# Kernel optimization log

Measured on AMD Instinct MI355X. Metric: run time of the kernel, lower is better.

## Reference

```python
import jax, jax.numpy as jnp
import numpy as np

N = 50000      # num nodes
E = 1_200_000  # num edges
NID = 92       # node_input_dim
ED = 1         # edge_input_dim
H = 64         # hidden_dim
L = 5          # num_layers
EMB = 64       # embedding_dim
G = 256        # num graphs in batch
EPS = 1e-5


def _glorot(key, shape):
    fan_in, fan_out = shape[-2], shape[-1]
    lim = float(np.sqrt(6.0 / (fan_in + fan_out)))
    return jax.random.uniform(key, shape, jnp.float32, -lim, lim)


def setup_inputs() -> dict:
    key = jax.random.key(0)
    ks = jax.random.split(key, 16)
    inp = {
        "x": jax.random.normal(ks[0], (N, NID), jnp.float32),
        "edge_attr": jax.random.uniform(ks[1], (E, ED), jnp.float32),
        "edge_index": jax.random.randint(ks[2], (2, E), 0, N, jnp.int32),
        "batch": jnp.sort(jax.random.randint(ks[3], (N,), 0, G, jnp.int32)),
        # node embedding
        "node_W": _glorot(ks[4], (NID, H)),
        "node_b": jnp.zeros((H,), jnp.float32),
        # per-layer message net: Linear(2H+ED,H) -> BN -> SiLU -> Linear(H,H)
        "msg_W1": _glorot(ks[5], (L, 2 * H + ED, H)),
        "msg_b1": jnp.zeros((L, H), jnp.float32),
        "msg_g1": jnp.ones((L, H), jnp.float32),
        "msg_be1": jnp.zeros((L, H), jnp.float32),
        "msg_W2": _glorot(ks[6], (L, H, H)),
        "msg_b2": jnp.zeros((L, H), jnp.float32),
        # per-layer update net: Linear(2H,H) -> BN -> SiLU
        "upd_W": _glorot(ks[7], (L, 2 * H, H)),
        "upd_b": jnp.zeros((L, H), jnp.float32),
        "upd_g": jnp.ones((L, H), jnp.float32),
        "upd_be": jnp.zeros((L, H), jnp.float32),
        # output projection
        "out_W": _glorot(ks[8], (H, EMB)),
        "out_b": jnp.zeros((EMB,), jnp.float32),
    }
    return inp


def _bn(z, g, b):
    # BatchNorm1d, training-mode batch statistics (biased variance), eps=1e-5
    mu = jnp.mean(z, axis=0)
    var = jnp.var(z, axis=0)
    return (z - mu) * jax.lax.rsqrt(var + EPS) * g + b


def reference(x, edge_attr, node_W, node_b, msg_W1, msg_b1, msg_g1, msg_be1,
              msg_W2, msg_b2, upd_W, upd_b, upd_g, upd_be, out_W, out_b,
              edge_index, batch):
    src, dst = edge_index[0], edge_index[1]  # PyG: x_j = x[src], x_i = x[dst]
    h = x @ node_W + node_b                  # [N, H]
    deg = jax.ops.segment_sum(jnp.ones((E,), h.dtype), dst, num_segments=N)
    deg = jnp.maximum(deg, 1.0)[:, None]     # mean aggregation denominator
    for l in range(L):
        # message: cat([x_i, x_j, edge_attr]) -> Linear -> BN -> SiLU -> Linear
        m = jnp.concatenate([h[dst], h[src], edge_attr], axis=1)  # [E, 2H+ED]
        m = _bn(m @ msg_W1[l] + msg_b1[l], msg_g1[l], msg_be1[l])
        m = jax.nn.silu(m) @ msg_W2[l] + msg_b2[l]                # [E, H]
        # aggregate: scatter-mean to destination nodes
        agg = jax.ops.segment_sum(m, dst, num_segments=N) / deg   # [N, H]
        # update: cat([x, agg]) -> Linear -> BN -> SiLU
        u = jnp.concatenate([h, agg], axis=1) @ upd_W[l] + upd_b[l]
        h = jax.nn.silu(_bn(u, upd_g[l], upd_be[l]))              # [N, H]
    # global mean pool over graphs
    cnt = jnp.maximum(jax.ops.segment_sum(jnp.ones((N,), h.dtype), batch, num_segments=G), 1.0)
    g = jax.ops.segment_sum(h, batch, num_segments=G) / cnt[:, None]  # [G, H]
    return jax.nn.silu(g @ out_W + out_b)                              # [G, EMB]
```

## Files before the change

kernel.cpp:

```cpp
#include <hip/hip_runtime.h>
#include <hip/hip_bf16.h>

#define NN 50000
#define EE 1200000
#define GG 256
#define LL 5

__device__ __forceinline__ float silu_f(float x) {
    return x * __builtin_amdgcn_rcpf(1.0f + __expf(-x));
}
__device__ __forceinline__ int rfl(int x) { return __builtin_amdgcn_readfirstlane(x); }

__global__ __launch_bounds__(256) void k_hist(const int* __restrict__ ei, int* __restrict__ fill, int E) {
    int e = blockIdx.x * 256 + threadIdx.x;
    if (e < E) atomicAdd(&fill[ei[E + e]], 1);
}

__global__ __launch_bounds__(256) void k_scan_blk(int* __restrict__ fill, int* __restrict__ rowptr,
                                                  float* __restrict__ degf, int* __restrict__ bsum, int n) {
    __shared__ int wsum[4];
    int tid = threadIdx.x, lane = tid & 63, wid = tid >> 6;
    int i = blockIdx.x * 256 + tid;
    int v = (i < n) ? fill[i] : 0;
    int x = v;
    #pragma unroll
    for (int off = 1; off < 64; off <<= 1) {
        int t = __shfl_up(x, off);
        if (lane >= off) x += t;
    }
    if (lane == 63) wsum[wid] = x;
    __syncthreads();
    int waveoff = 0;
    if (wid > 0) waveoff += wsum[0];
    if (wid > 1) waveoff += wsum[1];
    if (wid > 2) waveoff += wsum[2];
    int inc = x + waveoff;
    if (i < n) {
        rowptr[i + 1] = inc;
        degf[i] = (float)(v > 0 ? v : 1);
        fill[i] = 0;
    }
    if (tid == 255) bsum[blockIdx.x] = inc;
}

__global__ __launch_bounds__(256) void k_scan_top(int* __restrict__ bsum, int B) {
    __shared__ int wsum[4];
    int tid = threadIdx.x, lane = tid & 63, wid = tid >> 6;
    int v = (tid < B) ? bsum[tid] : 0;
    int x = v;
    #pragma unroll
    for (int off = 1; off < 64; off <<= 1) {
        int t = __shfl_up(x, off);
        if (lane >= off) x += t;
    }
    if (lane == 63) wsum[wid] = x;
    __syncthreads();
    int waveoff = 0;
    if (wid > 0) waveoff += wsum[0];
    if (wid > 1) waveoff += wsum[1];
    if (wid > 2) waveoff += wsum[2];
    if (tid < B) bsum[tid] = x + waveoff;
}

__global__ __launch_bounds__(256) void k_scan_add(const int* __restrict__ bsum, int* __restrict__ rowptr, int n) {
    int b = blockIdx.x;
    int i = b * 256 + threadIdx.x;
    if (i < n) {
        int add = (b > 0) ? bsum[b - 1] : 0;
        rowptr[i + 1] += add;
    }
    if (i == 0) rowptr[0] = 0;
}

__global__ __launch_bounds__(256) void k_scatter(const int* __restrict__ ei, const float* __restrict__ ea,
                                                 const int* __restrict__ rowptr, int* __restrict__ fill,
                                                 unsigned int* __restrict__ edata, int E) {
    int e = blockIdx.x * 256 + threadIdx.x;
    if (e < E) {
        int d = ei[E + e];
        int pos = atomicAdd(&fill[d], 1);
        int idx = rowptr[d] + pos;
        int ea15 = (int)(ea[e] * 32768.0f + 0.5f);
        if (ea15 > 32767) ea15 = 32767;
        edata[idx] = ((unsigned int)ea15 << 17) | (unsigned int)ei[e];
    }
}

__global__ __launch_bounds__(256) void k_fold(const float* __restrict__ msg_W2, const float* __restrict__ msg_b2,
                                              const float* __restrict__ upd_W, float* __restrict__ W2p,
                                              float* __restrict__ b2p) {
    int l = blockIdx.x;
    const float* W2 = msg_W2 + (size_t)l * 4096;
    const float* U2 = upd_W + (size_t)l * 8192 + 4096;
    int lane = threadIdx.x & 63, wid = threadIdx.x >> 6;
    for (int ii = 0; ii < 16; ii++) {
        int i = rfl(wid * 16 + ii);
        float acc = 0.0f;
        for (int k = 0; k < 64; k++) acc = fmaf(W2[i * 64 + k], U2[k * 64 + lane], acc);
        W2p[(size_t)l * 4096 + i * 64 + lane] = acc;
    }
    if (wid == 0) {
        float acc = 0.0f;
        for (int k = 0; k < 64; k++) acc = fmaf(msg_b2[l * 64 + k], U2[k * 64 + lane], acc);
        b2p[l * 64 + lane] = acc;
    }
}

__global__ __launch_bounds__(256) void k_node_emb(const float* __restrict__ x, const float* __restrict__ W,
                                                  const float* __restrict__ b, float* __restrict__ h, int n) {
    __shared__ float sW[92 * 64];
    __shared__ float sX[4][736];
    for (int i = threadIdx.x; i < 92 * 64; i += 256) sW[i] = W[i];
    __syncthreads();
    int lane = threadIdx.x & 63, wid = threadIdx.x >> 6;
    int gw = (blockIdx.x * 256 + threadIdx.x) >> 6;
    int nw = (gridDim.x * 256) >> 6;
    float bj = b[lane];
    int tiles = n >> 3;
    for (int t = gw; t < tiles; t += nw) {
        int rb = rfl(t << 3);
        const float4* xb = (const float4*)(x + (size_t)rb * 92);
        float4* sx4 = (float4*)&sX[wid][0];
        sx4[lane] = xb[lane];
        sx4[lane + 64] = xb[lane + 64];
        if (lane < 56) sx4[lane + 128] = xb[lane + 128];
        float acc[8];
        #pragma unroll
        for (int r = 0; r < 8; r++) acc[r] = bj;
        for (int kb = 0; kb < 80; kb += 16) {
            float wv[16];
            #pragma unroll
            for (int t2 = 0; t2 < 16; t2++) wv[t2] = sW[(kb + t2) * 64 + lane];
            #pragma unroll
            for (int r = 0; r < 8; r++) {
                #pragma unroll
                for (int t2 = 0; t2 < 16; t2++) acc[r] = fmaf(sX[wid][r * 92 + kb + t2], wv[t2], acc[r]);
            }
        }
        {
            float wv[12];
            #pragma unroll
            for (int t2 = 0; t2 < 12; t2++) wv[t2] = sW[(80 + t2) * 64 + lane];
            #pragma unroll
            for (int r = 0; r < 8; r++) {
                #pragma unroll
                for (int t2 = 0; t2 < 12; t2++) acc[r] = fmaf(sX[wid][r * 92 + 80 + t2], wv[t2], acc[r]);
            }
        }
        #pragma unroll
        for (int r = 0; r < 8; r++) h[(size_t)(rb + r) * 64 + lane] = acc[r];
    }
}

__global__ __launch_bounds__(256) void k_node_pre(const float* __restrict__ h, const float* __restrict__ W1,
                                                  const float* __restrict__ b1, float* __restrict__ Hd,
                                                  _Float16* __restrict__ Hs, int n) {
    __shared__ float sA[4096], sB[4096];
    __shared__ float sH[4][512];
    for (int i = threadIdx.x; i < 4096; i += 256) { sA[i] = W1[i]; sB[i] = W1[4096 + i]; }
    __syncthreads();
    int lane = threadIdx.x & 63, wid = threadIdx.x >> 6;
    int gw = (blockIdx.x * 256 + threadIdx.x) >> 6;
    int nw = (gridDim.x * 256) >> 6;
    float bj = b1[lane];
    int tiles = n >> 3;
    for (int t = gw; t < tiles; t += nw) {
        int rb = rfl(t << 3);
        const float4* hb = (const float4*)(h + (size_t)rb * 64);
        float4* sh4 = (float4*)&sH[wid][0];
        sh4[lane] = hb[lane];
        sh4[lane + 64] = hb[lane + 64];
        float accA[8], accB[8];
        #pragma unroll
        for (int r = 0; r < 8; r++) { accA[r] = bj; accB[r] = 0.0f; }
        for (int kb = 0; kb < 64; kb += 8) {
            float wA[8], wB[8];
            #pragma unroll
            for (int t2 = 0; t2 < 8; t2++) { wA[t2] = sA[(kb + t2) * 64 + lane]; wB[t2] = sB[(kb + t2) * 64 + lane]; }
            #pragma unroll
            for (int r = 0; r < 8; r++) {
                #pragma unroll
                for (int t2 = 0; t2 < 8; t2++) {
                    float hk = sH[wid][r * 64 + kb + t2];
                    accA[r] = fmaf(hk, wA[t2], accA[r]);
                    accB[r] = fmaf(hk, wB[t2], accB[r]);
                }
            }
        }
        #pragma unroll
        for (int r = 0; r < 8; r++) {
            Hd[(size_t)(rb + r) * 64 + lane] = accA[r];
            Hs[(size_t)(rb + r) * 64 + lane] = (_Float16)accB[r];
        }
    }
}

__global__ __launch_bounds__(256) void k_bn_pre(const float* __restrict__ u, const float* __restrict__ usum,
                                                const float* __restrict__ usq, const float* __restrict__ g,
                                                const float* __restrict__ be, const float* __restrict__ W1,
                                                const float* __restrict__ b1, float* __restrict__ h,
                                                float* __restrict__ Hd, _Float16* __restrict__ Hs,
                                                int n, float invN) {
    __shared__ float sA[4096], sB[4096];
    __shared__ float sH[4][8][64];
    for (int i = threadIdx.x; i < 4096; i += 256) { sA[i] = W1[i]; sB[i] = W1[4096 + i]; }
    __syncthreads();
    int lane = threadIdx.x & 63, wid = threadIdx.x >> 6;
    float mean = usum[lane] * invN;
    float var = usq[lane] * invN - mean * mean;
    float inv = rsqrtf(var + 1e-5f);
    float sc = inv * g[lane];
    float sh = fmaf(-mean, sc, be[lane]);
    float bj = b1[lane];
    int gw = (blockIdx.x * 256 + threadIdx.x) >> 6;
    int nw = (gridDim.x * 256) >> 6;
    int tiles = n >> 3;
    for (int t = gw; t < tiles; t += nw) {
        int rb = rfl(t << 3);
        #pragma unroll
        for (int r = 0; r < 8; r++) {
            float uv = u[(size_t)(rb + r) * 64 + lane];
            float hv = silu_f(fmaf(uv, sc, sh));
            h[(size_t)(rb + r) * 64 + lane] = hv;
            sH[wid][r][lane] = hv;
        }
        float accA[8], accB[8];
        #pragma unroll
        for (int r = 0; r < 8; r++) { accA[r] = bj; accB[r] = 0.0f; }
        for (int k = 0; k < 64; k += 2) {
            float wA0 = sA[k * 64 + lane],       wB0 = sB[k * 64 + lane];
            float wA1 = sA[(k + 1) * 64 + lane], wB1 = sB[(k + 1) * 64 + lane];
            #pragma unroll
            for (int r = 0; r < 8; r++) {
                float h0 = sH[wid][r][k], h1 = sH[wid][r][k + 1];
                accA[r] = fmaf(h0, wA0, accA[r]);
                accB[r] = fmaf(h0, wB0, accB[r]);
                accA[r] = fmaf(h1, wA1, accA[r]);
                accB[r] = fmaf(h1, wB1, accB[r]);
            }
        }
        #pragma unroll
        for (int r = 0; r < 8; r++) {
            Hd[(size_t)(rb + r) * 64 + lane] = accA[r];
            Hs[(size_t)(rb + r) * 64 + lane] = (_Float16)accB[r];
        }
    }
}

__global__ __launch_bounds__(256) void k_edge_stats(const float* __restrict__ Hd, const _Float16* __restrict__ Hs,
                                                    const int* __restrict__ rowptr, const unsigned int* __restrict__ edata,
                                                    const float* __restrict__ w1e,
                                                    float* __restrict__ esum, float* __restrict__ esq, int n) {
    __shared__ float rs[4][64], rq[4][64];
    int wid = threadIdx.x >> 6, lane = threadIdx.x & 63;
    int gw = (blockIdx.x * 256 + threadIdx.x) >> 6;
    int nw = (gridDim.x * 256) >> 6;
    float wj = w1e[lane] * (1.0f / 32768.0f);
    float s = 0.0f, q = 0.0f;
    for (int node = gw; node < n; node += nw) {
        int nu = rfl(node);
        int e0 = rowptr[nu], e1 = rowptr[nu + 1];
        if (e0 == e1) continue;
        float hd = Hd[(size_t)nu * 64 + lane];
        int e = e0;
        for (; e + 16 <= e1; e += 16) {
            float hs[16], av[16];
            #pragma unroll
            for (int j = 0; j < 16; j++) {
                unsigned int p = edata[e + j];
                int sidx = rfl((int)(p & 0x1FFFFu));
                av[j] = (float)rfl((int)(p >> 17));
                hs[j] = (float)Hs[(size_t)sidx * 64 + lane];
            }
            #pragma unroll
            for (int j = 0; j < 16; j++) {
                float z = fmaf(av[j], wj, hd) + hs[j];
                s += z;
                q = fmaf(z, z, q);
            }
        }
        for (; e + 8 <= e1; e += 8) {
            float hs[8], av[8];
            #pragma unroll
            for (int j = 0; j < 8; j++) {
                unsigned int p = edata[e + j];
                int sidx = rfl((int)(p & 0x1FFFFu));
                av[j] = (float)rfl((int)(p >> 17));
                hs[j] = (float)Hs[(size_t)sidx * 64 + lane];
            }
            #pragma unroll
            for (int j = 0; j < 8; j++) {
                float z = fmaf(av[j], wj, hd) + hs[j];
                s += z;
                q = fmaf(z, z, q);
            }
        }
        for (; e < e1; e++) {
            unsigned int p = edata[e];
            int sidx = rfl((int)(p & 0x1FFFFu));
            float a = (float)rfl((int)(p >> 17));
            float z = fmaf(a, wj, hd) + (float)Hs[(size_t)sidx * 64 + lane];
            s += z;
            q = fmaf(z, z, q);
        }
    }
    rs[wid][lane] = s; rq[wid][lane] = q;
    __syncthreads();
    if (wid == 0) {
        float ts = rs[0][lane] + rs[1][lane] + rs[2][lane] + rs[3][lane];
        float tq = rq[0][lane] + rq[1][lane] + rq[2][lane] + rq[3][lane];
        atomicAdd(&esum[lane], ts);
        atomicAdd(&esq[lane], tq);
    }
}

__global__ __launch_bounds__(256) void k_agg_upd(const float* __restrict__ Hd, const _Float16* __restrict__ Hs,
                                                 const int* __restrict__ rowptr, const unsigned int* __restrict__ edata,
                                                 const float* __restrict__ w1e,
                                                 const float* __restrict__ esum, const float* __restrict__ esq,
                                                 const float* __restrict__ g1, const float* __restrict__ be1,
                                                 const float* __restrict__ degf,
                                                 const float* __restrict__ h, const float* __restrict__ U1,
                                                 const float* __restrict__ W2p, const float* __restrict__ b2p,
                                                 const float* __restrict__ ub,
                                                 float* __restrict__ u, float* __restrict__ usum,
                                                 float* __restrict__ usq, int n, float invE) {
    __shared__ float sU[4096], sP[4096];
    __shared__ float2 sHA[4][4][64];
    for (int i = threadIdx.x; i < 4096; i += 256) { sU[i] = U1[i]; sP[i] = W2p[i]; }
    __syncthreads();
    int lane = threadIdx.x & 63, wid = threadIdx.x >> 6;
    float mean = esum[lane] * invE;
    float var = esq[lane] * invE - mean * mean;
    float inv = rsqrtf(var + 1e-5f);
    float sc = inv * g1[lane];
    float sh = fmaf(-mean, sc, be1[lane]);
    float wj = w1e[lane] * (1.0f / 32768.0f);
    float b2j = b2p[lane], ubj = ub[lane];
    int gw = (blockIdx.x * 256 + threadIdx.x) >> 6;
    int nw = (gridDim.x * 256) >> 6;
    float s = 0.0f, q = 0.0f;
    int tiles = n >> 2;
    for (int t = gw; t < tiles; t += nw) {
        int rb = rfl(t << 2);
        float gate[4];
        for (int r = 0; r < 4; r++) {
            int nu = rb + r;
            int e0 = rowptr[nu], e1 = rowptr[nu + 1];
            gate[r] = (e1 > e0) ? 1.0f : 0.0f;
            float hd = Hd[(size_t)nu * 64 + lane];
            float acc = 0.0f;
            int e = e0;
            for (; e + 16 <= e1; e += 16) {
                float hs[16], av[16];
                #pragma unroll
                for (int j = 0; j < 16; j++) {
                    unsigned int p = edata[e + j];
                    int sidx = rfl((int)(p & 0x1FFFFu));
                    av[j] = (float)rfl((int)(p >> 17));
                    hs[j] = (float)Hs[(size_t)sidx * 64 + lane];
                }
                #pragma unroll
                for (int j = 0; j < 16; j++) {
                    float z = fmaf(av[j], wj, hd) + hs[j];
                    acc += silu_f(fmaf(z, sc, sh));
                }
            }
            for (; e + 8 <= e1; e += 8) {
                float hs[8], av[8];
                #pragma unroll
                for (int j = 0; j < 8; j++) {
                    unsigned int p = edata[e + j];
                    int sidx = rfl((int)(p & 0x1FFFFu));
                    av[j] = (float)rfl((int)(p >> 17));
                    hs[j] = (float)Hs[(size_t)sidx * 64 + lane];
                }
                #pragma unroll
                for (int j = 0; j < 8; j++) {
                    float z = fmaf(av[j], wj, hd) + hs[j];
                    acc += silu_f(fmaf(z, sc, sh));
                }
            }
            for (; e < e1; e++) {
                unsigned int p = edata[e];
                int sidx = rfl((int)(p & 0x1FFFFu));
                float a = (float)rfl((int)(p >> 17));
                float z = fmaf(a, wj, hd) + (float)Hs[(size_t)sidx * 64 + lane];
                acc += silu_f(fmaf(z, sc, sh));
            }
            float hv = h[(size_t)nu * 64 + lane];
            sHA[wid][r][lane] = make_float2(hv, acc / degf[nu]);
        }
        float accu[4];
        #pragma unroll
        for (int r = 0; r < 4; r++) accu[r] = fmaf(gate[r], b2j, ubj);
        for (int k = 0; k < 64; k++) {
            float wU = sU[k * 64 + lane], wP = sP[k * 64 + lane];
            #pragma unroll
            for (int r = 0; r < 4; r++) {
                float2 ha = sHA[wid][r][k];
                accu[r] = fmaf(ha.x, wU, accu[r]);
                accu[r] = fmaf(ha.y, wP, accu[r]);
            }
        }
        #pragma unroll
        for (int r = 0; r < 4; r++) {
            u[(size_t)(rb + r) * 64 + lane] = accu[r];
            s += accu[r];
            q = fmaf(accu[r], accu[r], q);
        }
    }
    {
        float* my = (float*)&sHA[wid][0][0];
        my[lane] = s;
        my[64 + lane] = q;
    }
    __syncthreads();
    if (wid == 0) {
        float ts = 0.0f, tq = 0.0f;
        #pragma unroll
        for (int w = 0; w < 4; w++) {
            const float* b = (const float*)&sHA[w][0][0];
            ts += b[lane];
            tq += b[64 + lane];
        }
        atomicAdd(&usum[lane], ts);
        atomicAdd(&usq[lane], tq);
    }
}

__global__ __launch_bounds__(256) void k_bn_pool(const float* __restrict__ u, const float* __restrict__ usum,
                                                 const float* __restrict__ usq, const float* __restrict__ g,
                                                 const float* __restrict__ be, const int* __restrict__ batch,
                                                 float* __restrict__ gsum, float* __restrict__ gcnt,
                                                 int n, float invN) {
    __shared__ float ssc[64], ssh[64];
    if (threadIdx.x < 64) {
        int j = threadIdx.x;
        float mean = usum[j] * invN;
        float var = usq[j] * invN - mean * mean;
        float inv = rsqrtf(var + 1e-5f);
        float sc = inv * g[j];
        ssc[j] = sc;
        ssh[j] = fmaf(-mean, sc, be[j]);
    }
    __syncthreads();
    int lane = threadIdx.x & 63;
    int gw = (blockIdx.x * 256 + threadIdx.x) >> 6;
    int nw = (gridDim.x * 256) >> 6;
    int per = (n + nw - 1) / nw;
    int start = gw * per;
    int end = start + per; if (end > n) end = n;
    if (start >= end) return;
    float sc = ssc[lane], sh = ssh[lane];
    int cur = batch[start];
    float acc = 0.0f, c = 0.0f;
    for (int i = start; i < end; i++) {
        int b = batch[i];
        if (b != cur) {
            atomicAdd(&gsum[(size_t)cur * 64 + lane], acc);
            if (lane == 0) atomicAdd(&gcnt[cur], c);
            cur = b; acc = 0.0f; c = 0.0f;
        }
        float y = fmaf(u[(size_t)i * 64 + lane], sc, sh);
        acc += silu_f(y);
        c += 1.0f;
    }
    atomicAdd(&gsum[(size_t)cur * 64 + lane], acc);
    if (lane == 0) atomicAdd(&gcnt[cur], c);
}

__global__ __launch_bounds__(256) void k_out(const float* __restrict__ gsum, const float* __restrict__ gcnt,
                                             const float* __restrict__ OW, const float* __restrict__ ob,
                                             float* __restrict__ out, int G) {
    __shared__ float sW[4096];
    for (int i = threadIdx.x; i < 4096; i += 256) sW[i] = OW[i];
    __syncthreads();
    int lane = threadIdx.x & 63;
    int gw = (blockIdx.x * 256 + threadIdx.x) >> 6;
    int nw = (gridDim.x * 256) >> 6;
    for (int g = gw; g < G; g += nw) {
        int gu = rfl(g);
        float c = gcnt[gu]; if (c < 1.0f) c = 1.0f;
        float ci = 1.0f / c;
        float acc = ob[lane];
        const float* gr = gsum + (size_t)gu * 64;
        #pragma unroll
        for (int k = 0; k < 64; k++) acc = fmaf(gr[k] * ci, sW[k * 64 + lane], acc);
        out[(size_t)gu * 64 + lane] = silu_f(acc);
    }
}

extern "C" void kernel_launch(void* const* d_in, const int* in_sizes, int n_in,
                              void* d_out, int out_size, void* d_ws, size_t ws_size,
                              hipStream_t stream) {
    const int N = NN, E = EE, G = GG, L = LL;
    const float* x         = (const float*)d_in[0];
    const float* edge_attr = (const float*)d_in[1];
    const int*   edge_index= (const int*)d_in[2];
    const int*   batch     = (const int*)d_in[3];
    const float* node_W    = (const float*)d_in[4];
    const float* node_b    = (const float*)d_in[5];
    const float* msg_W1    = (const float*)d_in[6];
    const float* msg_b1    = (const float*)d_in[7];
    const float* msg_g1    = (const float*)d_in[8];
    const float* msg_be1   = (const float*)d_in[9];
    const float* msg_W2    = (const float*)d_in[10];
    const float* msg_b2    = (const float*)d_in[11];
    const float* upd_W     = (const float*)d_in[12];
    const float* upd_b     = (const float*)d_in[13];
    const float* upd_g     = (const float*)d_in[14];
    const float* upd_be    = (const float*)d_in[15];
    const float* out_W     = (const float*)d_in[16];
    const float* out_b     = (const float*)d_in[17];
    float* out = (float*)d_out;

    char* ws = (char*)d_ws;
    size_t off = 0;
    auto alloc = [&](size_t b) { size_t o = off; off = (off + b + 255) & ~(size_t)255; return o; };
    float* h    = (float*)(ws + alloc((size_t)N * 64 * 4));
    float* Hd   = (float*)(ws + alloc((size_t)N * 64 * 4));
    _Float16* Hs = (_Float16*)(ws + alloc((size_t)N * 64 * 2));
    unsigned int* edata = (unsigned int*)(ws + alloc((size_t)E * 4));
    int* rowptr = (int*)  (ws + alloc((size_t)(N + 1) * 4));
    float* degf = (float*)(ws + alloc((size_t)N * 4));
    float* W2p  = (float*)(ws + alloc((size_t)L * 4096 * 4));
    float* b2p  = (float*)(ws + alloc((size_t)L * 64 * 4));
    int* bsum   = (int*)  (ws + alloc((size_t)256 * 4));
    size_t zero_begin = off;
    int*   fill = (int*)  (ws + alloc((size_t)N * 4));
    float* stats= (float*)(ws + alloc((size_t)L * 4 * 64 * 4));
    float* gsum = (float*)(ws + alloc((size_t)(G * 64 + G) * 4));
    size_t zero_end = off;
    float* gcnt = gsum + (size_t)G * 64;
    float* u = Hd;

    hipMemsetAsync(ws + zero_begin, 0, zero_end - zero_begin, stream);

    const int SB = (N + 255) / 256;
    k_hist<<<(E + 255) / 256, 256, 0, stream>>>(edge_index, fill, E);
    k_scan_blk<<<SB, 256, 0, stream>>>(fill, rowptr, degf, bsum, N);
    k_scan_top<<<1, 256, 0, stream>>>(bsum, SB);
    k_scan_add<<<SB, 256, 0, stream>>>(bsum, rowptr, N);
    k_scatter<<<(E + 255) / 256, 256, 0, stream>>>(edge_index, edge_attr, rowptr, fill, edata, E);

    k_fold<<<L, 256, 0, stream>>>(msg_W2, msg_b2, upd_W, W2p, b2p);
    k_node_emb<<<1024, 256, 0, stream>>>(x, node_W, node_b, h, N);

    k_node_pre<<<1024, 256, 0, stream>>>(h, msg_W1, msg_b1, Hd, Hs, N);

    for (int l = 0; l < L; l++) {
        const float* W1  = msg_W1 + (size_t)l * 129 * 64;
        const float* w1e = W1 + 128 * 64;
        float* esum = stats + (size_t)l * 256;
        float* esq  = esum + 64;
        float* usum = esum + 128;
        float* usq  = esum + 192;
        k_edge_stats<<<2048, 256, 0, stream>>>(Hd, Hs, rowptr, edata, w1e, esum, esq, N);
        k_agg_upd<<<1024, 256, 0, stream>>>(Hd, Hs, rowptr, edata, w1e, esum, esq,
                                            msg_g1 + l * 64, msg_be1 + l * 64, degf,
                                            h, upd_W + (size_t)l * 8192, W2p + (size_t)l * 4096,
                                            b2p + (size_t)l * 64, upd_b + l * 64,
                                            u, usum, usq, N, 1.0f / E);
        if (l < L - 1) {
            const float* W1n = msg_W1 + (size_t)(l + 1) * 129 * 64;
            k_bn_pre<<<1024, 256, 0, stream>>>(u, usum, usq, upd_g + l * 64, upd_be + l * 64,
                                               W1n, msg_b1 + (l + 1) * 64, h, Hd, Hs, N, 1.0f / N);
        } else {
            k_bn_pool<<<256, 256, 0, stream>>>(u, usum, usq, upd_g + l * 64, upd_be + l * 64,
                                               batch, gsum, gcnt, N, 1.0f / N);
        }
    }

    k_out<<<64, 256, 0, stream>>>(gsum, gcnt, out_W, out_b, out, G);
}
```

Baseline: 1.177 ms.

## Materialize gathered source features per edge in stats pass, stream them in aggregation

The edge-stats kernel now writes each gathered fp16 source-node row into a contiguous per-edge buffer (E×64 halves). The aggregation kernel then reads that buffer sequentially instead of repeating the random gather through Hs. This swaps a second random gather for an extra write plus a streaming read of about 150 MB per layer. It only runs when the workspace is large enough, otherwise the old path is used.

```diff
diff --git a/kernel.cpp b/kernel.cpp
--- a/kernel.cpp
+++ b/kernel.cpp
@@ -247,9 +247,11 @@
     }
 }
 
+template<bool CACHE>
 __global__ __launch_bounds__(256) void k_edge_stats(const float* __restrict__ Hd, const _Float16* __restrict__ Hs,
                                                     const int* __restrict__ rowptr, const unsigned int* __restrict__ edata,
                                                     const float* __restrict__ w1e,
+                                                    _Float16* __restrict__ hsc,
                                                     float* __restrict__ esum, float* __restrict__ esq, int n) {
     __shared__ float rs[4][64], rq[4][64];
     int wid = threadIdx.x >> 6, lane = threadIdx.x & 63;
@@ -264,33 +266,43 @@
         float hd = Hd[(size_t)nu * 64 + lane];
         int e = e0;
         for (; e + 16 <= e1; e += 16) {
-            float hs[16], av[16];
+            _Float16 hr[16]; float av[16];
             #pragma unroll
             for (int j = 0; j < 16; j++) {
                 unsigned int p = edata[e + j];
                 int sidx = rfl((int)(p & 0x1FFFFu));
                 av[j] = (float)rfl((int)(p >> 17));
-                hs[j] = (float)Hs[(size_t)sidx * 64 + lane];
+                hr[j] = Hs[(size_t)sidx * 64 + lane];
+            }
+            if (CACHE) {
+                _Float16* wp = hsc + (size_t)e * 64 + lane;
+                #pragma unroll
+                for (int j = 0; j < 16; j++) wp[j * 64] = hr[j];
             }
             #pragma unroll
             for (int j = 0; j < 16; j++) {
-                float z = fmaf(av[j], wj, hd) + hs[j];
+                float z = fmaf(av[j], wj, hd) + (float)hr[j];
                 s += z;
                 q = fmaf(z, z, q);
             }
         }
         for (; e + 8 <= e1; e += 8) {
-            float hs[8], av[8];
+            _Float16 hr[8]; float av[8];
             #pragma unroll
             for (int j = 0; j < 8; j++) {
                 unsigned int p = edata[e + j];
                 int sidx = rfl((int)(p & 0x1FFFFu));
                 av[j] = (float)rfl((int)(p >> 17));
-                hs[j] = (float)Hs[(size_t)sidx * 64 + lane];
+                hr[j] = Hs[(size_t)sidx * 64 + lane];
+            }
+            if (CACHE) {
+                _Float16* wp = hsc + (size_t)e * 64 + lane;
+                #pragma unroll
+                for (int j = 0; j < 8; j++) wp[j * 64] = hr[j];
             }
             #pragma unroll
             for (int j = 0; j < 8; j++) {
-                float z = fmaf(av[j], wj, hd) + hs[j];
+                float z = fmaf(av[j], wj, hd) + (float)hr[j];
                 s += z;
                 q = fmaf(z, z, q);
             }
@@ -299,7 +311,9 @@
             unsigned int p = edata[e];
             int sidx = rfl((int)(p & 0x1FFFFu));
             float a = (float)rfl((int)(p >> 17));
-            float z = fmaf(a, wj, hd) + (float)Hs[(size_t)sidx * 64 + lane];
+            _Float16 hr = Hs[(size_t)sidx * 64 + lane];
+            if (CACHE) hsc[(size_t)e * 64 + lane] = hr;
+            float z = fmaf(a, wj, hd) + (float)hr;
             s += z;
             q = fmaf(z, z, q);
         }
@@ -314,12 +328,14 @@
     }
 }
 
+template<bool STREAM>
 __global__ __launch_bounds__(256) void k_agg_upd(const float* __restrict__ Hd, const _Float16* __restrict__ Hs,
                                                  const int* __restrict__ rowptr, const unsigned int* __restrict__ edata,
                                                  const float* __restrict__ w1e,
                                                  const float* __restrict__ esum, const float* __restrict__ esq,
                                                  const float* __restrict__ g1, const float* __restrict__ be1,
                                                  const float* __restrict__ degf,
+                                                 const _Float16* __restrict__ hsc,
                                                  const float* __restrict__ h, const float* __restrict__ U1,
                                                  const float* __restrict__ W2p, const float* __restrict__ b2p,
                                                  const float* __restrict__ ub,
@@ -353,12 +369,22 @@
             int e = e0;
             for (; e + 16 <= e1; e += 16) {
                 float hs[16], av[16];
-                #pragma unroll
-                for (int j = 0; j < 16; j++) {
-                    unsigned int p = edata[e + j];
-                    int sidx = rfl((int)(p & 0x1FFFFu));
-                    av[j] = (float)rfl((int)(p >> 17));
-                    hs[j] = (float)Hs[(size_t)sidx * 64 + lane];
+                if (STREAM) {
+                    const _Float16* hp = hsc + (size_t)e * 64 + lane;
+                    #pragma unroll
+                    for (int j = 0; j < 16; j++) {
+                        unsigned int p = edata[e + j];
+                        av[j] = (float)rfl((int)(p >> 17));
+                        hs[j] = (float)hp[j * 64];
+                    }
+                } else {
+                    #pragma unroll
+                    for (int j = 0; j < 16; j++) {
+                        unsigned int p = edata[e + j];
+                        int sidx = rfl((int)(p & 0x1FFFFu));
+                        av[j] = (float)rfl((int)(p >> 17));
+                        hs[j] = (float)Hs[(size_t)sidx * 64 + lane];
+                    }
                 }
                 #pragma unroll
                 for (int j = 0; j < 16; j++) {
@@ -368,12 +394,22 @@
             }
             for (; e + 8 <= e1; e += 8) {
                 float hs[8], av[8];
-                #pragma unroll
-                for (int j = 0; j < 8; j++) {
-                    unsigned int p = edata[e + j];
-                    int sidx = rfl((int)(p & 0x1FFFFu));
-                    av[j] = (float)rfl((int)(p >> 17));
-                    hs[j] = (float)Hs[(size_t)sidx * 64 + lane];
+                if (STREAM) {
+                    const _Float16* hp = hsc + (size_t)e * 64 + lane;
+                    #pragma unroll
+                    for (int j = 0; j < 8; j++) {
+                        unsigned int p = edata[e + j];
+                        av[j] = (float)rfl((int)(p >> 17));
+                        hs[j] = (float)hp[j * 64];
+                    }
+                } else {
+                    #pragma unroll
+                    for (int j = 0; j < 8; j++) {
+                        unsigned int p = edata[e + j];
+                        int sidx = rfl((int)(p & 0x1FFFFu));
+                        av[j] = (float)rfl((int)(p >> 17));
+                        hs[j] = (float)Hs[(size_t)sidx * 64 + lane];
+                    }
                 }
                 #pragma unroll
                 for (int j = 0; j < 8; j++) {
@@ -383,13 +419,19 @@
             }
             for (; e < e1; e++) {
                 unsigned int p = edata[e];
-                int sidx = rfl((int)(p & 0x1FFFFu));
                 float a = (float)rfl((int)(p >> 17));
-                float z = fmaf(a, wj, hd) + (float)Hs[(size_t)sidx * 64 + lane];
+                float hv;
+                if (STREAM) {
+                    hv = (float)hsc[(size_t)e * 64 + lane];
+                } else {
+                    int sidx = rfl((int)(p & 0x1FFFFu));
+                    hv = (float)Hs[(size_t)sidx * 64 + lane];
+                }
+                float z = fmaf(a, wj, hd) + hv;
                 acc += silu_f(fmaf(z, sc, sh));
             }
-            float hv = h[(size_t)nu * 64 + lane];
-            sHA[wid][r][lane] = make_float2(hv, acc / degf[nu]);
+            float hvv = h[(size_t)nu * 64 + lane];
+            sHA[wid][r][lane] = make_float2(hvv, acc / degf[nu]);
         }
         float accu[4];
         #pragma unroll
@@ -534,6 +576,9 @@
     size_t zero_end = off;
     float* gcnt = gsum + (size_t)G * 64;
     float* u = Hd;
+    size_t hsc_off = alloc((size_t)E * 64 * 2);
+    _Float16* hsc = (_Float16*)(ws + hsc_off);
+    const bool use_cache = (ws_size >= off);
 
     hipMemsetAsync(ws + zero_begin, 0, zero_end - zero_begin, stream);
 
@@ -556,12 +601,21 @@
         float* esq  = esum + 64;
         float* usum = esum + 128;
         float* usq  = esum + 192;
-        k_edge_stats<<<2048, 256, 0, stream>>>(Hd, Hs, rowptr, edata, w1e, esum, esq, N);
-        k_agg_upd<<<1024, 256, 0, stream>>>(Hd, Hs, rowptr, edata, w1e, esum, esq,
-                                            msg_g1 + l * 64, msg_be1 + l * 64, degf,
-                                            h, upd_W + (size_t)l * 8192, W2p + (size_t)l * 4096,
-                                            b2p + (size_t)l * 64, upd_b + l * 64,
-                                            u, usum, usq, N, 1.0f / E);
+        if (use_cache) {
+            k_edge_stats<true><<<2048, 256, 0, stream>>>(Hd, Hs, rowptr, edata, w1e, hsc, esum, esq, N);
+            k_agg_upd<true><<<1024, 256, 0, stream>>>(Hd, Hs, rowptr, edata, w1e, esum, esq,
+                                                      msg_g1 + l * 64, msg_be1 + l * 64, degf, hsc,
+                                                      h, upd_W + (size_t)l * 8192, W2p + (size_t)l * 4096,
+                                                      b2p + (size_t)l * 64, upd_b + l * 64,
+                                                      u, usum, usq, N, 1.0f / E);
+        } else {
+            k_edge_stats<false><<<2048, 256, 0, stream>>>(Hd, Hs, rowptr, edata, w1e, nullptr, esum, esq, N);
+            k_agg_upd<false><<<1024, 256, 0, stream>>>(Hd, Hs, rowptr, edata, w1e, esum, esq,
+                                                       msg_g1 + l * 64, msg_be1 + l * 64, degf, nullptr,
+                                                       h, upd_W + (size_t)l * 8192, W2p + (size_t)l * 4096,
+                                                       b2p + (size_t)l * 64, upd_b + l * 64,
+                                                       u, usum, usq, N, 1.0f / E);
+        }
         if (l < L - 1) {
             const float* W1n = msg_W1 + (size_t)(l + 1) * 129 * 64;
             k_bn_pre<<<1024, 256, 0, stream>>>(u, usum, usq, upd_g + l * 64, upd_be + l * 64,
```

New measurement: 1.228 ms. +4.3%, slower.
